# Kernel tuning notes

Hardware: AMD Instinct MI355X
Metric: run time of the kernel (lower is better)

## Reference

```python
import jax, jax.numpy as jnp
import numpy as np

N_NODES = 100000
N_EDGES = 3200000
IN_CH = 256
HID = 256   # 2 * out_channels
OUT = 128


def _gcn_norm(edge_index, n):
    # PyG GCNConv normalization: add self-loops, norm = d^-1/2[src] * d^-1/2[dst]
    src, dst = edge_index[0], edge_index[1]
    loops = jnp.arange(n, dtype=src.dtype)
    src = jnp.concatenate([src, loops])
    dst = jnp.concatenate([dst, loops])
    ones = jnp.ones_like(dst, dtype=jnp.float32)
    deg = jax.ops.segment_sum(ones, dst, num_segments=n)
    dinv = jnp.where(deg > 0, jax.lax.rsqrt(deg), 0.0)
    norm = dinv[src] * dinv[dst]
    return src, dst, norm


def _gcn_conv(x, W, b, src, dst, norm, n):
    h = x @ W                              # [N, F_out] dense transform first (F_out <= F_in)
    msg = h[src] * norm[:, None]           # gather + scale  [E+N, F_out]
    out = jax.ops.segment_sum(msg, dst, num_segments=n)  # scatter-add
    return out + b


def setup_inputs() -> dict:
    key = jax.random.key(0)
    k1, k2, k3, k4 = jax.random.split(key, 4)
    x = jax.random.normal(k1, (N_NODES, IN_CH), dtype=jnp.float32)
    edge_index = jax.random.randint(k2, (2, N_EDGES), 0, N_NODES, dtype=jnp.int64)
    # Glorot-style init for weights, zero bias (PyG GCNConv defaults)
    W1 = jax.random.normal(k3, (IN_CH, HID), dtype=jnp.float32) * (1.0 / np.sqrt(IN_CH))
    b1 = jnp.zeros((HID,), dtype=jnp.float32)
    W2 = jax.random.normal(k4, (HID, OUT), dtype=jnp.float32) * (1.0 / np.sqrt(HID))
    b2 = jnp.zeros((OUT,), dtype=jnp.float32)
    return {"x": x, "edge_index": edge_index, "W1": W1, "b1": b1, "W2": W2, "b2": b2}


def reference(x, edge_index, W1, b1, W2, b2):
    n = x.shape[0]
    src, dst, norm = _gcn_norm(edge_index, n)  # cached=True: shared across both layers
    h = _gcn_conv(x, W1, b1, src, dst, norm, n)
    h = jax.nn.relu(h)
    z = _gcn_conv(h, W2, b2, src, dst, norm, n)
    return z
```

## Files before the change

kernel.cpp:

```cpp
#include <hip/hip_runtime.h>
#include <cstdio>


#define NPB 256
#define PCHUNK 8192

template <int V> struct vec_t;
template <> struct vec_t<2> {
  typedef float    fv __attribute__((ext_vector_type(2)));
  typedef _Float16 hv __attribute__((ext_vector_type(2)));
};
template <> struct vec_t<4> {
  typedef float    fv __attribute__((ext_vector_type(4)));
  typedef _Float16 hv __attribute__((ext_vector_type(4)));
};
typedef _Float16 half4v __attribute__((ext_vector_type(4)));
typedef _Float16 half8v __attribute__((ext_vector_type(8)));
typedef float    f32x4  __attribute__((ext_vector_type(4)));

__global__ __launch_bounds__(256) void k_zero(int* p, int n) {
  int i = blockIdx.x * 256 + threadIdx.x;
  if (i < n) p[i] = 0;
}

__global__ __launch_bounds__(256) void k_bhist(const int* __restrict__ dst,
                                               int* __restrict__ bcnt,
                                               int e, int nb) {
  __shared__ int h[512];
  for (int i = threadIdx.x; i < nb; i += 256) h[i] = 0;
  __syncthreads();
  int c0 = blockIdx.x * PCHUNK;
  int c1 = min(c0 + PCHUNK, e);
  for (int i = c0 + threadIdx.x; i < c1; i += 256)
    atomicAdd(&h[dst[i] >> 8], 1);
  __syncthreads();
  for (int i = threadIdx.x; i < nb; i += 256)
    if (h[i]) atomicAdd(&bcnt[i], h[i]);
}

__global__ __launch_bounds__(512) void k_bscan(const int* __restrict__ bcnt,
                                               int* __restrict__ bbase,
                                               int* __restrict__ gcur, int nb) {
  __shared__ int sm[512];
  int tid = threadIdx.x;
  sm[tid] = (tid < nb) ? bcnt[tid] : 0;
  __syncthreads();
  for (int d = 1; d < 512; d <<= 1) {
    int t = (tid >= d) ? sm[tid - d] : 0;
    __syncthreads();
    sm[tid] += t;
    __syncthreads();
  }
  int ex = (tid == 0) ? 0 : sm[tid - 1];
  if (tid < nb) {
    bbase[tid] = ex;
    gcur[tid] = ex;
  }
  if (tid == nb) bbase[nb] = sm[nb - 1];
}

__global__ __launch_bounds__(256) void k_partition(const int* __restrict__ src,
                                                   const int* __restrict__ dst,
                                                   int* __restrict__ gcur,
                                                   uint2* __restrict__ tmp,
                                                   int e, int nb) {
  __shared__ int hist[512];
  __shared__ int base[512];
  for (int i = threadIdx.x; i < nb; i += 256) hist[i] = 0;
  __syncthreads();
  int c0 = blockIdx.x * PCHUNK;
  int c1 = min(c0 + PCHUNK, e);
  for (int i = c0 + threadIdx.x; i < c1; i += 256)
    atomicAdd(&hist[dst[i] >> 8], 1);
  __syncthreads();
  for (int i = threadIdx.x; i < nb; i += 256) {
    int c = hist[i];
    base[i] = c ? atomicAdd(&gcur[i], c) : 0;
    hist[i] = 0;
  }
  __syncthreads();
  for (int i = c0 + threadIdx.x; i < c1; i += 256) {
    int d = dst[i];
    int b = d >> 8;
    int pos = base[b] + atomicAdd(&hist[b], 1);
    uint2 v;
    v.x = (unsigned)src[i];
    v.y = (unsigned)d;
    tmp[pos] = v;
  }
}

__global__ __launch_bounds__(256) void k_bucket(const uint2* __restrict__ tmp,
                                                const int* __restrict__ bbase,
                                                int* __restrict__ off,
                                                float* __restrict__ dinv,
                                                int* __restrict__ esrc, int n) {
  __shared__ int lcnt[NPB];
  __shared__ int lsum[NPB];
  __shared__ int lcur[NPB];
  const int b = blockIdx.x;
  const int tid = threadIdx.x;
  const int r0 = b << 8;
  const int nn = min(NPB, n - r0);
  const int lo = bbase[b], hi = bbase[b + 1];

  lcnt[tid] = 0;
  __syncthreads();
  for (int i = lo + tid; i < hi; i += 256)
    atomicAdd(&lcnt[tmp[i].y & (NPB - 1)], 1);
  __syncthreads();
  lsum[tid] = lcnt[tid];
  __syncthreads();
  for (int d = 1; d < NPB; d <<= 1) {
    int t = (tid >= d) ? lsum[tid - d] : 0;
    __syncthreads();
    lsum[tid] += t;
    __syncthreads();
  }
  int ex = (tid == 0) ? 0 : lsum[tid - 1];
  if (tid < nn) {
    off[r0 + tid] = lo + ex;
    dinv[r0 + tid] = rsqrtf((float)(lcnt[tid] + 1));
    lcur[tid] = lo + ex;
  }
  if (r0 + nn == n && tid == 0) off[n] = hi;
  __syncthreads();
  for (int i = lo + tid; i < hi; i += 256) {
    uint2 t2 = tmp[i];
    int pos = atomicAdd(&lcur[t2.y & (NPB - 1)], 1);
    esrc[pos] = (int)t2.x;
  }
}

__global__ __launch_bounds__(256) void k_castWT(const float* __restrict__ W,
                                                _Float16* __restrict__ WhT,
                                                _Float16* __restrict__ WlT,
                                                int K, int N) {
  int i = blockIdx.x * 256 + threadIdx.x;
  if (i >= K * N) return;
  int n = i % N, k = i / N;
  float v = W[i];
  _Float16 h = (_Float16)v;
  WhT[(size_t)n * K + k] = h;
  WlT[(size_t)n * K + k] = (_Float16)(v - (float)h);
}

template <typename AT, int NTERMS>
__global__ __launch_bounds__(256, 2) void k_gemm_mfma(
    const AT* __restrict__ A, const _Float16* __restrict__ BhT,
    const _Float16* __restrict__ BlT, _Float16* __restrict__ C,
    int M, int N, int K) {
  constexpr bool SPLITA = (NTERMS == 3);
  __shared__ _Float16 Ah[128][40];
  __shared__ _Float16 Al[SPLITA ? 128 : 1][40];

  const int tid = threadIdx.x;
  const int bm = blockIdx.x * 128;
  const int bn = blockIdx.y * 128;

  const int arow = tid >> 1;
  const int acol = (tid & 1) * 16;
  const bool avalid = (bm + arow) < M;
  const AT* aptr = A + (size_t)(bm + arow) * K + acol;

  const int wave = tid >> 6, lane = tid & 63;
  const int wm = (wave & 1) * 64, wn = (wave >> 1) * 64;
  const int lr = lane & 15, quad = lane >> 4;

  const _Float16* bh0 = BhT + (size_t)(bn + wn + lr) * K + quad * 8;
  const _Float16* bl0 = BlT + (size_t)(bn + wn + lr) * K + quad * 8;

  f32x4 acc[4][4] = {};

  for (int k0 = 0; k0 < K; k0 += 32) {
    __syncthreads();
    if (avalid) {
#pragma unroll
      for (int ii = 0; ii < 4; ++ii) {
        if constexpr (SPLITA) {
          f32x4 v = *(const f32x4*)(aptr + k0 + ii * 4);
          half4v hv, lv;
#pragma unroll
          for (int j = 0; j < 4; ++j) {
            hv[j] = (_Float16)v[j];
            lv[j] = (_Float16)(v[j] - (float)hv[j]);
          }
          *(half4v*)&Ah[arow][acol + ii * 4] = hv;
          *(half4v*)&Al[arow][acol + ii * 4] = lv;
        } else {
          half4v v = *(const half4v*)(aptr + k0 + ii * 4);
          *(half4v*)&Ah[arow][acol + ii * 4] = v;
        }
      }
    } else {
      half4v z = {};
#pragma unroll
      for (int ii = 0; ii < 4; ++ii) {
        *(half4v*)&Ah[arow][acol + ii * 4] = z;
        if constexpr (SPLITA) *(half4v*)&Al[arow][acol + ii * 4] = z;
      }
    }
    __syncthreads();

    half8v af[4], alf[4], bhf[4], blf[4];
#pragma unroll
    for (int mi = 0; mi < 4; ++mi) {
      af[mi] = *(const half8v*)&Ah[wm + mi * 16 + lr][quad * 8];
      if constexpr (SPLITA)
        alf[mi] = *(const half8v*)&Al[wm + mi * 16 + lr][quad * 8];
    }
#pragma unroll
    for (int ni = 0; ni < 4; ++ni) {
      bhf[ni] = *(const half8v*)(bh0 + (size_t)(ni * 16) * K + k0);
      blf[ni] = *(const half8v*)(bl0 + (size_t)(ni * 16) * K + k0);
    }
#pragma unroll
    for (int mi = 0; mi < 4; ++mi)
#pragma unroll
      for (int ni = 0; ni < 4; ++ni) {
        acc[mi][ni] = __builtin_amdgcn_mfma_f32_16x16x32_f16(
            af[mi], bhf[ni], acc[mi][ni], 0, 0, 0);
        acc[mi][ni] = __builtin_amdgcn_mfma_f32_16x16x32_f16(
            af[mi], blf[ni], acc[mi][ni], 0, 0, 0);
        if constexpr (SPLITA)
          acc[mi][ni] = __builtin_amdgcn_mfma_f32_16x16x32_f16(
              alf[mi], bhf[ni], acc[mi][ni], 0, 0, 0);
      }
  }

#pragma unroll
  for (int mi = 0; mi < 4; ++mi)
#pragma unroll
    for (int r = 0; r < 4; ++r) {
      int row = bm + wm + mi * 16 + quad * 4 + r;
      if (row < M) {
#pragma unroll
        for (int ni = 0; ni < 4; ++ni)
          C[(size_t)row * N + bn + wn + ni * 16 + lr] =
              (_Float16)acc[mi][ni][r];
      }
    }
}

template <int C, bool RELU, typename OutT>
__global__ __launch_bounds__(256) void k_agg(const _Float16* __restrict__ h,
                                             const int* __restrict__ esrc,
                                             const int* __restrict__ off,
                                             const float* __restrict__ dinv,
                                             const float* __restrict__ bias,
                                             OutT* __restrict__ out, int n) {
  constexpr int V = C / 64;
  typedef typename vec_t<V>::fv FV;
  typedef typename vec_t<V>::hv HV;
  int gwave = (blockIdx.x * 256 + threadIdx.x) >> 6;
  int lane = threadIdx.x & 63;
  if (gwave >= n) return;
  const int i = gwave;
  const float di = dinv[i];

  FV acc = di * __builtin_convertvector(
                    *(const HV*)(h + (size_t)i * C + lane * V), FV);

  int e = off[i];
  const int e1 = off[i + 1];
  for (; e + 3 < e1; e += 4) {
    int s0 = esrc[e], s1 = esrc[e + 1], s2 = esrc[e + 2], s3 = esrc[e + 3];
    float w0 = dinv[s0], w1 = dinv[s1], w2 = dinv[s2], w3 = dinv[s3];
    HV v0 = *(const HV*)(h + (size_t)s0 * C + lane * V);
    HV v1 = *(const HV*)(h + (size_t)s1 * C + lane * V);
    HV v2 = *(const HV*)(h + (size_t)s2 * C + lane * V);
    HV v3 = *(const HV*)(h + (size_t)s3 * C + lane * V);
    acc += w0 * __builtin_convertvector(v0, FV);
    acc += w1 * __builtin_convertvector(v1, FV);
    acc += w2 * __builtin_convertvector(v2, FV);
    acc += w3 * __builtin_convertvector(v3, FV);
  }
  for (; e < e1; ++e) {
    int s = esrc[e];
    acc += dinv[s] * __builtin_convertvector(
                         *(const HV*)(h + (size_t)s * C + lane * V), FV);
  }

  FV bv = *(const FV*)(bias + lane * V);
  FV r = acc * di + bv;
  if (RELU) {
#pragma unroll
    for (int v = 0; v < V; ++v) r[v] = fmaxf(r[v], 0.f);
  }
  if constexpr (sizeof(OutT) == 2) {
    *(HV*)(out + (size_t)i * C + lane * V) = __builtin_convertvector(r, HV);
  } else {
    *(FV*)(out + (size_t)i * C + lane * V) = r;
  }
}

extern "C" void kernel_launch(void* const* d_in, const int* in_sizes, int n_in,
                              void* d_out, int out_size, void* d_ws, size_t ws_size,
                              hipStream_t stream) {
  const float* x  = (const float*)d_in[0];
  const int*   ei = (const int*)d_in[1];
  const float* W1 = (const float*)d_in[2];
  const float* b1 = (const float*)d_in[3];
  const float* W2 = (const float*)d_in[4];
  const float* b2 = (const float*)d_in[5];
  float* out = (float*)d_out;

  const int IN_CH = 256, HID = 256, OUT = 128;
  const int N = in_sizes[0] / IN_CH;
  const int E = in_sizes[1] / 2;
  const int* src = ei;
  const int* dst = ei + E;
  const int NB = (N + NPB - 1) / NPB;

  char* p = (char*)d_ws;
  auto alloc = [&](size_t bytes) {
    void* r = (void*)p;
    p += (bytes + 255) & ~(size_t)255;
    return r;
  };
  _Float16* h1   = (_Float16*)alloc((size_t)N * HID * 2);
  _Float16* h1r  = (_Float16*)alloc((size_t)N * HID * 2);
  int*      esrc = (int*)alloc((size_t)E * 4);
  uint2*    tmp  = (uint2*)alloc((size_t)E * 8);
  int*      off  = (int*)alloc((size_t)(N + 1) * 4);
  float*    dinv = (float*)alloc((size_t)N * 4);
  int*      bcnt = (int*)alloc((size_t)(NB + 1) * 4);
  int*      bbase= (int*)alloc((size_t)(NB + 1) * 4);
  int*      gcur = (int*)alloc((size_t)(NB + 1) * 4);
  _Float16* w1h  = (_Float16*)alloc((size_t)IN_CH * HID * 2);
  _Float16* w1l  = (_Float16*)alloc((size_t)IN_CH * HID * 2);
  _Float16* w2h  = (_Float16*)alloc((size_t)HID * OUT * 2);
  _Float16* w2l  = (_Float16*)alloc((size_t)HID * OUT * 2);
  if ((size_t)(p - (char*)d_ws) > ws_size) {
    fprintf(stderr, "kernel_launch: ws too small (need %zu, have %zu)\n",
            (size_t)(p - (char*)d_ws), ws_size);
    return;
  }

  const int nBlkP = (E + PCHUNK - 1) / PCHUNK;

  k_zero<<<(NB + 255) / 256, 256, 0, stream>>>(bcnt, NB);
  k_bhist<<<nBlkP, 256, 0, stream>>>(dst, bcnt, E, NB);
  k_bscan<<<1, 512, 0, stream>>>(bcnt, bbase, gcur, NB);
  k_partition<<<nBlkP, 256, 0, stream>>>(src, dst, gcur, tmp, E, NB);
  k_bucket<<<NB, 256, 0, stream>>>(tmp, bbase, off, dinv, esrc, N);
  k_castWT<<<(IN_CH * HID + 255) / 256, 256, 0, stream>>>(W1, w1h, w1l, IN_CH, HID);
  k_castWT<<<(HID * OUT + 255) / 256, 256, 0, stream>>>(W2, w2h, w2l, HID, OUT);
  dim3 g1((N + 127) / 128, HID / 128);
  k_gemm_mfma<float, 3><<<g1, 256, 0, stream>>>(x, w1h, w1l, h1, N, HID, IN_CH);
  int aggBlk = (N + 3) / 4;
  k_agg<256, true, _Float16><<<aggBlk, 256, 0, stream>>>(h1, esrc, off, dinv, b1, h1r, N);
  dim3 g2((N + 127) / 128, OUT / 128);
  k_gemm_mfma<_Float16, 2><<<g2, 256, 0, stream>>>(h1r, w2h, w2l, h1, N, OUT, HID);
  k_agg<128, false, float><<<aggBlk, 256, 0, stream>>>(h1, esrc, off, dinv, b2, out, N);
}
```

Baseline: 743.1 us.

## Split wave across edges with 16-byte gathers and shuffle reduction in aggregation

```diff
diff --git a/kernel.cpp b/kernel.cpp
--- a/kernel.cpp
+++ b/kernel.cpp
@@ -5,18 +5,10 @@
 #define NPB 256
 #define PCHUNK 8192
 
-template <int V> struct vec_t;
-template <> struct vec_t<2> {
-  typedef float    fv __attribute__((ext_vector_type(2)));
-  typedef _Float16 hv __attribute__((ext_vector_type(2)));
-};
-template <> struct vec_t<4> {
-  typedef float    fv __attribute__((ext_vector_type(4)));
-  typedef _Float16 hv __attribute__((ext_vector_type(4)));
-};
 typedef _Float16 half4v __attribute__((ext_vector_type(4)));
 typedef _Float16 half8v __attribute__((ext_vector_type(8)));
 typedef float    f32x4  __attribute__((ext_vector_type(4)));
+typedef float    f32x8  __attribute__((ext_vector_type(8)));
 
 __global__ __launch_bounds__(256) void k_zero(int* p, int n) {
   int i = blockIdx.x * 256 + threadIdx.x;
@@ -249,48 +241,70 @@
                                              const float* __restrict__ dinv,
                                              const float* __restrict__ bias,
                                              OutT* __restrict__ out, int n) {
-  constexpr int V = C / 64;
-  typedef typename vec_t<V>::fv FV;
-  typedef typename vec_t<V>::hv HV;
+  constexpr int LPE = C / 8;
+  constexpr int EPL = 64 / LPE;
+  constexpr int U = 4;
   int gwave = (blockIdx.x * 256 + threadIdx.x) >> 6;
   int lane = threadIdx.x & 63;
   if (gwave >= n) return;
   const int i = gwave;
+  const int eslot = lane / LPE;
+  const int sub = lane % LPE;
   const float di = dinv[i];
-
-  FV acc = di * __builtin_convertvector(
-                    *(const HV*)(h + (size_t)i * C + lane * V), FV);
+  const _Float16* hb = h + sub * 8;
+
+  f32x8 acc = {};
+  if (eslot == 0)
+    acc = di * __builtin_convertvector(*(const half8v*)(hb + (size_t)i * C),
+                                       f32x8);
 
   int e = off[i];
   const int e1 = off[i + 1];
-  for (; e + 3 < e1; e += 4) {
-    int s0 = esrc[e], s1 = esrc[e + 1], s2 = esrc[e + 2], s3 = esrc[e + 3];
-    float w0 = dinv[s0], w1 = dinv[s1], w2 = dinv[s2], w3 = dinv[s3];
-    HV v0 = *(const HV*)(h + (size_t)s0 * C + lane * V);
-    HV v1 = *(const HV*)(h + (size_t)s1 * C + lane * V);
-    HV v2 = *(const HV*)(h + (size_t)s2 * C + lane * V);
-    HV v3 = *(const HV*)(h + (size_t)s3 * C + lane * V);
-    acc += w0 * __builtin_convertvector(v0, FV);
-    acc += w1 * __builtin_convertvector(v1, FV);
-    acc += w2 * __builtin_convertvector(v2, FV);
-    acc += w3 * __builtin_convertvector(v3, FV);
-  }
-  for (; e < e1; ++e) {
-    int s = esrc[e];
-    acc += dinv[s] * __builtin_convertvector(
-                         *(const HV*)(h + (size_t)s * C + lane * V), FV);
-  }
-
-  FV bv = *(const FV*)(bias + lane * V);
-  FV r = acc * di + bv;
-  if (RELU) {
-#pragma unroll
-    for (int v = 0; v < V; ++v) r[v] = fmaxf(r[v], 0.f);
-  }
-  if constexpr (sizeof(OutT) == 2) {
-    *(HV*)(out + (size_t)i * C + lane * V) = __builtin_convertvector(r, HV);
-  } else {
-    *(FV*)(out + (size_t)i * C + lane * V) = r;
+  for (; e + U * EPL <= e1; e += U * EPL) {
+    int s[U];
+#pragma unroll
+    for (int g = 0; g < U; ++g) s[g] = esrc[e + g * EPL + eslot];
+    float w[U];
+    half8v v[U];
+#pragma unroll
+    for (int g = 0; g < U; ++g) {
+      w[g] = dinv[s[g]];
+      v[g] = *(const half8v*)(hb + (size_t)s[g] * C);
+    }
+#pragma unroll
+    for (int g = 0; g < U; ++g)
+      acc += w[g] * __builtin_convertvector(v[g], f32x8);
+  }
+  for (; e < e1; e += EPL) {
+    int eg = e + eslot;
+    if (eg < e1) {
+      int s = esrc[eg];
+      acc += dinv[s] * __builtin_convertvector(
+                           *(const half8v*)(hb + (size_t)s * C), f32x8);
+    }
+  }
+
+#pragma unroll
+  for (int j = 0; j < 8; ++j) {
+    float t = acc[j];
+    if constexpr (EPL >= 4) t += __shfl_xor(t, 16);
+    t += __shfl_xor(t, 32);
+    acc[j] = t;
+  }
+
+  if (eslot == 0) {
+    f32x8 bv = *(const f32x8*)(bias + sub * 8);
+    f32x8 r = acc * di + bv;
+    if (RELU) {
+#pragma unroll
+      for (int j = 0; j < 8; ++j) r[j] = fmaxf(r[j], 0.f);
+    }
+    if constexpr (sizeof(OutT) == 2) {
+      *(half8v*)(out + (size_t)i * C + sub * 8) =
+          __builtin_convertvector(r, half8v);
+    } else {
+      *(f32x8*)(out + (size_t)i * C + sub * 8) = r;
+    }
   }
 }
 
```

Measured after the change: 735.6 us. About the same (-1.0%).
